# Performance work log

Measured on AMD Instinct MI355X. Metric: run time of the kernel, lower is better.

Reference implementation:

```python
import jax, jax.numpy as jnp
import numpy as np

B, N, D, H, DH = 128, 128, 64, 8, 64
CBS = SBS = 4
NSEL, WIN = 2, 2
NB = N // CBS
NEG = -1e30


def _ln(x, g, b, eps=1e-5):
    mu = jnp.mean(x, -1, keepdims=True)
    var = jnp.mean((x - mu) ** 2, -1, keepdims=True)
    return (x - mu) * jax.lax.rsqrt(var + eps) * g + b


def _rms(x, g, eps=1e-6):
    return x * jax.lax.rsqrt(jnp.mean(x * x, -1, keepdims=True) + eps) * g


def _gelu(x):
    return jax.nn.gelu(x, approximate=False)


def setup_inputs() -> dict:
    key = jax.random.key(0)
    ks = iter(jax.random.split(key, 40))
    def rn(shape, s=0.05):
        return jax.random.normal(next(ks), shape, jnp.float32) * s
    return dict(
        x=jax.random.normal(next(ks), (B, N), jnp.float32),
        W_emb=rn((D,)), b_emb=rn((D,)),
        rms_scale=jnp.ones((D,), jnp.float32),
        Wq=rn((D, H * DH)), Wk=rn((D, H * DH)), Wv=rn((D, H * DH)),
        k_pos=rn((H, CBS, DH)), v_pos=rn((H, CBS, DH)),
        Wck=rn((CBS * DH, DH)), bck=rn((DH,)), Wcv=rn((CBS * DH, DH)), bcv=rn((DH,)),
        mem_ck=rn((H, 1, DH)), mem_cv=rn((H, 1, DH)),
        Wg=rn((D, 3 * H)), bg=rn((3 * H,)),
        Wo=rn((H * DH, D)),
        ln1_g=jnp.ones((D,), jnp.float32), ln1_b=jnp.zeros((D,), jnp.float32),
        Wt1=rn((N, 256)), bt1=rn((256,)), Wt2=rn((256, N)), bt2=rn((N,)),
        ln2_g=jnp.ones((D,), jnp.float32), ln2_b=jnp.zeros((D,), jnp.float32),
        Wc1=rn((D, 256)), bc1=rn((256,)), Wc2=rn((256, D)), bc2=rn((D,)),
        Wh1=rn((D, 32)), bh1=rn((32,)), Wh2=rn((32, 1)), bh2=rn((1,)),
    )


def reference(x, W_emb, b_emb, rms_scale, Wq, Wk, Wv, k_pos, v_pos, Wck, bck, Wcv, bcv,
              mem_ck, mem_cv, Wg, bg, Wo, ln1_g, ln1_b, Wt1, bt1, Wt2, bt2,
              ln2_g, ln2_b, Wc1, bc1, Wc2, bc2, Wh1, bh1, Wh2, bh2):
    scale = DH ** -0.5
    pos = jnp.arange(N)
    e = x[..., None] * W_emb + b_emb                         # [B,N,D] per-feature embedding (Linear(1,D))
    # ---- NSA sparse attention branch ----
    h = _rms(e, rms_scale)
    q = (h @ Wq).reshape(B, N, H, DH).transpose(0, 2, 1, 3)  # bhnd
    k = (h @ Wk).reshape(B, N, H, DH).transpose(0, 2, 1, 3)
    v = (h @ Wv).reshape(B, N, H, DH).transpose(0, 2, 1, 3)
    # compressed-block branch: intra-block pos emb + linear compression, 1 learned mem KV
    kb = k.reshape(B, H, NB, CBS, DH) + k_pos[None, :, None]
    vb = v.reshape(B, H, NB, CBS, DH) + v_pos[None, :, None]
    ck = kb.reshape(B, H, NB, CBS * DH) @ Wck + bck          # [B,H,NB,DH]
    cv = vb.reshape(B, H, NB, CBS * DH) @ Wcv + bcv
    ckm = jnp.concatenate([jnp.broadcast_to(mem_ck[None], (B, H, 1, DH)), ck], axis=2)
    cvm = jnp.concatenate([jnp.broadcast_to(mem_cv[None], (B, H, 1, DH)), cv], axis=2)
    cs = jnp.einsum('bhnd,bhjd->bhnj', q, ckm) * scale
    blk_end = (jnp.arange(NB) + 1) * CBS - 1                 # block fully in the past is visible
    cmask = jnp.concatenate([jnp.ones((N, 1), bool), pos[:, None] >= blk_end[None, :]], axis=1)
    cs = jnp.where(cmask[None, None], cs, NEG)
    out_c = jnp.einsum('bhnj,bhjd->bhnd', jax.nn.softmax(cs, -1), cvm)
    # fine branch: top-k selected blocks (by compressed scores) + forced causal diagonal block
    vals, sel = jax.lax.top_k(cs[..., 1:], NSEL)             # [B,H,N,NSEL]
    qblk = pos // SBS
    sel_ok = (vals > NEG / 2) & (sel != qblk[None, None, :, None])
    sel_tok = (sel[..., None] * SBS + jnp.arange(SBS)).reshape(B, H, N, NSEL * SBS)
    gather = jax.vmap(jax.vmap(lambda t, i: t[i]))           # per (b,h) token gather
    fk_sel = gather(k, sel_tok)
    fv_sel = gather(v, sel_tok)
    diag = qblk[:, None] * SBS + jnp.arange(SBS)             # [N,SBS]
    fk = jnp.concatenate([fk_sel, k[:, :, diag]], axis=3)    # [B,H,N,(NSEL+1)*SBS,DH]
    fv = jnp.concatenate([fv_sel, v[:, :, diag]], axis=3)
    fidx = jnp.concatenate([sel_tok, jnp.broadcast_to(diag[None, None], (B, H, N, SBS))], axis=3)
    fmask = (fidx <= pos[None, None, :, None]) & jnp.concatenate(
        [jnp.repeat(sel_ok, SBS, axis=-1), jnp.ones((B, H, N, SBS), bool)], axis=3)
    fs = jnp.where(fmask, jnp.einsum('bhnd,bhnsd->bhns', q, fk) * scale, NEG)
    out_f = jnp.einsum('bhns,bhnsd->bhnd', jax.nn.softmax(fs, -1), fv)
    offs = pos[:, None] - jnp.arange(WIN - 1, -1, -1)[None, :]
    oc = jnp.clip(offs, 0, None)
    wk = k[:, :, oc]
    wv = v[:, :, oc]
    ws = jnp.where((offs >= 0)[None, None], jnp.einsum('bhnd,bhnwd->bhnw', q, wk) * scale, NEG)
    out_w = jnp.einsum('bhnw,bhnwd->bhnd', jax.nn.softmax(ws, -1), wv)
    # per-head sigmoid 3-way strategy gates + output projection
    g = jax.nn.sigmoid(h @ Wg + bg).reshape(B, N, 3, H).transpose(0, 3, 2, 1)  # [B,H,3,N]
    attn = g[:, :, 0, :, None] * out_c + g[:, :, 1, :, None] * out_f + g[:, :, 2, :, None] * out_w
    x1 = attn.transpose(0, 2, 1, 3).reshape(B, N, H * DH) @ Wo
    # ---- TabMixer branch (token-mix over N, channel-mix over D) ----
    t = _ln(e, ln1_g, ln1_b).transpose(0, 2, 1)              # [B,D,N]
    m = e + (_gelu(t @ Wt1 + bt1) @ Wt2 + bt2).transpose(0, 2, 1)
    m = m + _gelu(_ln(m, ln2_g, ln2_b) @ Wc1 + bc1) @ Wc2 + bc2
    # ---- fuse, mean-pool over tokens, MLP head ----
    y = (x1 + m).mean(axis=1)
    return _gelu(y @ Wh1 + bh1) @ Wh2 + bh2                  # [B,1]
```

## Files before the change

kernel.cpp:

```cpp
#include <hip/hip_runtime.h>
#include <math.h>

#define B_ 128
#define N_ 128
#define D_ 64
#define H_ 8
#define DH_ 64
#define NEGF (-1e30f)

__device__ __forceinline__ float wred(float v) {
#pragma unroll
  for (int off = 32; off > 0; off >>= 1) v += __shfl_xor(v, off, 64);
  return v;
}

__device__ __forceinline__ float gelu_f(float x) {
  return 0.5f * x * (1.f + erff(x * 0.70710678118654752440f));
}

__global__ void __launch_bounds__(256) k2_embed_proj(
    const float* __restrict__ x, const float* __restrict__ Wemb,
    const float* __restrict__ bemb, const float* __restrict__ rmsg,
    const float* __restrict__ ln1g, const float* __restrict__ ln1b,
    const float* __restrict__ Wq, const float* __restrict__ Wk,
    const float* __restrict__ Wv, const float* __restrict__ Wg,
    const float* __restrict__ bg, float* __restrict__ e,
    float* __restrict__ lne, float* __restrict__ q,
    float* __restrict__ k, float* __restrict__ v, float* __restrict__ g) {
  __shared__ __align__(16) float hs[32 * 68];
  int tid = threadIdx.x;
  int r0 = blockIdx.x * 32;
  int chunk = blockIdx.y;
  int wave = tid >> 6, lane = tid & 63;
  for (int rr = 0; rr < 8; ++rr) {
    int r = wave * 8 + rr;
    int row = r0 + r;
    float xv = x[row];
    float ev = fmaf(xv, Wemb[lane], bemb[lane]);
    float ss = wred(ev * ev) * (1.f / 64.f);
    float hv = ev * rsqrtf(ss + 1e-6f) * rmsg[lane];
    float mu = wred(ev) * (1.f / 64.f);
    float dv = ev - mu;
    float var = wred(dv * dv) * (1.f / 64.f);
    if (chunk == 0) {
      float lv = dv * rsqrtf(var + 1e-5f) * ln1g[lane] + ln1b[lane];
      size_t o = (size_t)row * 64 + lane;
      e[o] = ev; lne[o] = lv;
    }
    hs[r * 68 + lane] = hv;
  }
  __syncthreads();
  const float* W = (chunk == 0) ? Wq : ((chunk == 1) ? Wk : Wv);
  float* dst = (chunk == 0) ? q : ((chunk == 1) ? k : v);
  {
    int tx = tid & 127, ty = tid >> 7;
    float4 acc[16];
#pragma unroll
    for (int r = 0; r < 16; ++r) acc[r] = make_float4(0.f, 0.f, 0.f, 0.f);
    const float* Wp = W + 4 * tx;
#pragma unroll 2
    for (int k4 = 0; k4 < 16; ++k4) {
      float4 w0 = *(const float4*)(Wp + (size_t)(4 * k4 + 0) * 512);
      float4 w1 = *(const float4*)(Wp + (size_t)(4 * k4 + 1) * 512);
      float4 w2 = *(const float4*)(Wp + (size_t)(4 * k4 + 2) * 512);
      float4 w3 = *(const float4*)(Wp + (size_t)(4 * k4 + 3) * 512);
#pragma unroll
      for (int r = 0; r < 16; ++r) {
        float4 hv = *(const float4*)&hs[(ty * 16 + r) * 68 + 4 * k4];
        acc[r].x = fmaf(hv.x, w0.x, fmaf(hv.y, w1.x, fmaf(hv.z, w2.x, fmaf(hv.w, w3.x, acc[r].x))));
        acc[r].y = fmaf(hv.x, w0.y, fmaf(hv.y, w1.y, fmaf(hv.z, w2.y, fmaf(hv.w, w3.y, acc[r].y))));
        acc[r].z = fmaf(hv.x, w0.z, fmaf(hv.y, w1.z, fmaf(hv.z, w2.z, fmaf(hv.w, w3.z, acc[r].z))));
        acc[r].w = fmaf(hv.x, w0.w, fmaf(hv.y, w1.w, fmaf(hv.z, w2.w, fmaf(hv.w, w3.w, acc[r].w))));
      }
    }
    int hh = (4 * tx) >> 6, d4 = (4 * tx) & 63;
    int bb = r0 >> 7;
    float* dbase = dst + ((size_t)(bb * 8 + hh) * 128) * 64 + d4;
#pragma unroll
    for (int r = 0; r < 16; ++r) {
      int nn = (r0 & 127) + ty * 16 + r;
      *(float4*)(dbase + (size_t)nn * 64) = acc[r];
    }
  }
  {
    int r = tid >> 3, gl = tid & 7;
    int gc = chunk * 8 + gl;
    float a = bg[gc];
#pragma unroll 4
    for (int k4 = 0; k4 < 16; ++k4) {
      float4 hv = *(const float4*)&hs[r * 68 + 4 * k4];
      a = fmaf(hv.x, Wg[(4 * k4 + 0) * 24 + gc],
          fmaf(hv.y, Wg[(4 * k4 + 1) * 24 + gc],
          fmaf(hv.z, Wg[(4 * k4 + 2) * 24 + gc],
          fmaf(hv.w, Wg[(4 * k4 + 3) * 24 + gc], a))));
    }
    g[(size_t)(r0 + r) * 24 + gc] = 1.f / (1.f + __expf(-a));
  }
}

__global__ void __launch_bounds__(256) k3_compress(
    const float* __restrict__ k, const float* __restrict__ v,
    const float* __restrict__ kpos, const float* __restrict__ vpos,
    const float* __restrict__ Wck, const float* __restrict__ bck,
    const float* __restrict__ Wcv, const float* __restrict__ bcv,
    const float* __restrict__ mck, const float* __restrict__ mcv,
    float* __restrict__ ckm, float* __restrict__ cvm) {
  __shared__ __align__(16) float sb[32 * 260];
  int bh = blockIdx.x; int hh = bh & 7;
  int tid = threadIdx.x;
  int tx = tid & 15, ty = tid >> 4;
  const float4* sb4 = (const float4*)sb;
  for (int pass = 0; pass < 2; ++pass) {
    const float* src = pass ? v : k;
    const float* pos = pass ? vpos : kpos;
    const float* Wc = pass ? Wcv : Wck;
    const float* bc = pass ? bcv : bck;
    const float* mc = pass ? mcv : mck;
    float* out = pass ? cvm : ckm;
    if (pass) __syncthreads();
    for (int idx = tid; idx < 8192; idx += 256) {
      int tok = idx >> 6, dd = idx & 63;
      sb[(tok >> 2) * 260 + (tok & 3) * 64 + dd] =
          src[(size_t)bh * 8192 + idx] + pos[(hh * 4 + (tok & 3)) * 64 + dd];
    }
    __syncthreads();
    float4 b4 = *(const float4*)(bc + 4 * tx);
    float4 a0 = b4, a1 = b4;
    const float* Wp = Wc + 4 * tx;
#pragma unroll 2
    for (int k4 = 0; k4 < 64; ++k4) {
      float4 w0 = *(const float4*)(Wp + (size_t)(4 * k4 + 0) * 64);
      float4 w1 = *(const float4*)(Wp + (size_t)(4 * k4 + 1) * 64);
      float4 w2 = *(const float4*)(Wp + (size_t)(4 * k4 + 2) * 64);
      float4 w3 = *(const float4*)(Wp + (size_t)(4 * k4 + 3) * 64);
      float4 s0 = sb4[ty * 65 + k4];
      float4 s1 = sb4[(ty + 16) * 65 + k4];
      a0.x = fmaf(s0.x, w0.x, fmaf(s0.y, w1.x, fmaf(s0.z, w2.x, fmaf(s0.w, w3.x, a0.x))));
      a0.y = fmaf(s0.x, w0.y, fmaf(s0.y, w1.y, fmaf(s0.z, w2.y, fmaf(s0.w, w3.y, a0.y))));
      a0.z = fmaf(s0.x, w0.z, fmaf(s0.y, w1.z, fmaf(s0.z, w2.z, fmaf(s0.w, w3.z, a0.z))));
      a0.w = fmaf(s0.x, w0.w, fmaf(s0.y, w1.w, fmaf(s0.z, w2.w, fmaf(s0.w, w3.w, a0.w))));
      a1.x = fmaf(s1.x, w0.x, fmaf(s1.y, w1.x, fmaf(s1.z, w2.x, fmaf(s1.w, w3.x, a1.x))));
      a1.y = fmaf(s1.x, w0.y, fmaf(s1.y, w1.y, fmaf(s1.z, w2.y, fmaf(s1.w, w3.y, a1.y))));
      a1.z = fmaf(s1.x, w0.z, fmaf(s1.y, w1.z, fmaf(s1.z, w2.z, fmaf(s1.w, w3.z, a1.z))));
      a1.w = fmaf(s1.x, w0.w, fmaf(s1.y, w1.w, fmaf(s1.z, w2.w, fmaf(s1.w, w3.w, a1.w))));
    }
    *(float4*)(out + ((size_t)bh * 33 + ty + 1) * 64 + 4 * tx) = a0;
    *(float4*)(out + ((size_t)bh * 33 + ty + 17) * 64 + 4 * tx) = a1;
    if (tid < 16) *(float4*)(out + (size_t)bh * 2112 + 4 * tid) = *(const float4*)(mc + hh * 64 + 4 * tid);
  }
}

#define KLD 68
__global__ void __launch_bounds__(128, 2) k4_attn(
    const float* __restrict__ q, const float* __restrict__ k, const float* __restrict__ v,
    const float* __restrict__ ckm, const float* __restrict__ cvm, const float* __restrict__ g,
    float* __restrict__ attn) {
  __shared__ __align__(16) float ks[128 * KLD];
  int bh = blockIdx.x; int b = bh >> 3, hh = bh & 7;
  int tid = threadIdx.x;
  for (int idx = tid; idx < 8192; idx += 128)
    ks[(idx >> 6) * KLD + (idx & 63)] = k[(size_t)bh * 8192 + idx];
  __syncthreads();
  const int n = tid;
  float4 qr[16];
  {
    const float4* q4 = (const float4*)(q + (size_t)bh * 8192 + (size_t)n * 64);
#pragma unroll
    for (int i = 0; i < 16; ++i) {
      float4 t = q4[i];
      t.x *= 0.125f; t.y *= 0.125f; t.z *= 0.125f; t.w *= 0.125f;
      qr[i] = t;
    }
  }
  auto dot = [&](const float4* __restrict__ rp) {
    float s0 = 0.f, s1 = 0.f;
#pragma unroll
    for (int i = 0; i < 16; i += 2) {
      float4 c0 = rp[i], c1 = rp[i + 1];
      s0 = fmaf(qr[i].x, c0.x, s0); s0 = fmaf(qr[i].y, c0.y, s0);
      s0 = fmaf(qr[i].z, c0.z, s0); s0 = fmaf(qr[i].w, c0.w, s0);
      s1 = fmaf(qr[i + 1].x, c1.x, s1); s1 = fmaf(qr[i + 1].y, c1.y, s1);
      s1 = fmaf(qr[i + 1].z, c1.z, s1); s1 = fmaf(qr[i + 1].w, c1.w, s1);
    }
    return s0 + s1;
  };
  const float* ck0 = ckm + (size_t)bh * 2112;
  const int jmax = (n + 1) >> 2;
  float scc[33];
#pragma unroll
  for (int j = 0; j < 33; ++j) {
    float s = dot((const float4*)(ck0 + j * 64));
    scc[j] = (j == 0 || j <= jmax) ? s : NEGF;
  }
  int i1 = 0; float b1 = scc[1];
#pragma unroll
  for (int j = 2; j < 33; ++j) {
    if (scc[j] > b1) { b1 = scc[j]; i1 = j - 1; }
  }
  int i2 = 0; float b2 = -3.0e38f;
#pragma unroll
  for (int j = 1; j < 33; ++j) {
    if ((j - 1 != i1) && (scc[j] > b2)) { b2 = scc[j]; i2 = j - 1; }
  }
  const int qb = n >> 2;
  const bool ok1 = (b1 > -5e29f) && (i1 != qb);
  const bool ok2 = (b2 > -5e29f) && (i2 != qb);
  const int row1 = i1 * 4, row2 = i2 * 4, rowd = qb * 4;
  float sf[12];
#pragma unroll
  for (int s2 = 0; s2 < 4; ++s2) {
    int t1 = row1 + s2;
    sf[s2] = (ok1 && t1 <= n) ? dot((const float4*)(ks + t1 * KLD)) : NEGF;
    int t2 = row2 + s2;
    sf[4 + s2] = (ok2 && t2 <= n) ? dot((const float4*)(ks + t2 * KLD)) : NEGF;
    int t3 = rowd + s2;
    sf[8 + s2] = (t3 <= n) ? dot((const float4*)(ks + t3 * KLD)) : NEGF;
  }
  float sw0 = (n >= 1) ? dot((const float4*)(ks + (n - 1) * KLD)) : NEGF;
  float sw1 = dot((const float4*)(ks + n * KLD));
  __syncthreads();
  for (int idx = tid; idx < 8192; idx += 128)
    ks[(idx >> 6) * KLD + (idx & 63)] = v[(size_t)bh * 8192 + idx];
  __syncthreads();
  float mxc = scc[0];
#pragma unroll
  for (int j = 1; j < 33; ++j) mxc = fmaxf(mxc, scc[j]);
  float denc = 0.f;
#pragma unroll
  for (int j = 0; j < 33; ++j) { float p = __expf(scc[j] - mxc); scc[j] = p; denc += p; }
  float mxf = sf[0];
#pragma unroll
  for (int i = 1; i < 12; ++i) mxf = fmaxf(mxf, sf[i]);
  float denf = 0.f;
#pragma unroll
  for (int i = 0; i < 12; ++i) { float p = __expf(sf[i] - mxf); sf[i] = p; denf += p; }
  float mxw = fmaxf(sw0, sw1);
  float pw0 = __expf(sw0 - mxw), pw1 = __expf(sw1 - mxw);
  const float* gr = g + (size_t)(b * 128 + n) * 24;
  float gc0 = gr[hh] / denc;
  float gf0 = gr[8 + hh] / denf;
  float gw0 = gr[16 + hh] / (pw0 + pw1);
  float pww0 = pw0 * gw0, pww1 = pw1 * gw0;
  int nm1 = (n >= 1) ? (n - 1) : 0;
  const float* cv0 = cvm + (size_t)bh * 2112;
  float4* arow = (float4*)(attn + ((size_t)(b * 128 + n)) * 512 + hh * 64);
  for (int h2 = 0; h2 < 2; ++h2) {
    float4 oa[8];
#pragma unroll
    for (int i = 0; i < 8; ++i) oa[i] = make_float4(0.f, 0.f, 0.f, 0.f);
#pragma unroll
    for (int j = 0; j < 33; ++j) {
      float p = scc[j] * gc0;
      const float4* cr = (const float4*)(cv0 + j * 64) + h2 * 8;
#pragma unroll
      for (int i = 0; i < 8; ++i) {
        float4 c = cr[i];
        oa[i].x = fmaf(p, c.x, oa[i].x); oa[i].y = fmaf(p, c.y, oa[i].y);
        oa[i].z = fmaf(p, c.z, oa[i].z); oa[i].w = fmaf(p, c.w, oa[i].w);
      }
    }
#pragma unroll
    for (int si = 0; si < 12; ++si) {
      int tok = ((si < 4) ? row1 : (si < 8) ? row2 : rowd) + (si & 3);
      float p = sf[si] * gf0;
      const float4* vr = (const float4*)(ks + tok * KLD) + h2 * 8;
#pragma unroll
      for (int i = 0; i < 8; ++i) {
        float4 c = vr[i];
        oa[i].x = fmaf(p, c.x, oa[i].x); oa[i].y = fmaf(p, c.y, oa[i].y);
        oa[i].z = fmaf(p, c.z, oa[i].z); oa[i].w = fmaf(p, c.w, oa[i].w);
      }
    }
    {
      const float4* v0 = (const float4*)(ks + nm1 * KLD) + h2 * 8;
      const float4* v1 = (const float4*)(ks + n * KLD) + h2 * 8;
#pragma unroll
      for (int i = 0; i < 8; ++i) {
        float4 c0 = v0[i], c1 = v1[i];
        oa[i].x = fmaf(pww0, c0.x, fmaf(pww1, c1.x, oa[i].x));
        oa[i].y = fmaf(pww0, c0.y, fmaf(pww1, c1.y, oa[i].y));
        oa[i].z = fmaf(pww0, c0.z, fmaf(pww1, c1.z, oa[i].z));
        oa[i].w = fmaf(pww0, c0.w, fmaf(pww1, c1.w, oa[i].w));
      }
    }
#pragma unroll
    for (int i = 0; i < 8; ++i) arow[h2 * 8 + i] = oa[i];
  }
}

__global__ void __launch_bounds__(256) k5_wo(const float* __restrict__ attn,
                                             const float* __restrict__ Wo,
                                             float* __restrict__ x1) {
  __shared__ __align__(16) float as[16 * 516];
  int tid = threadIdx.x;
  size_t base = (size_t)blockIdx.x * 8192;
  for (int idx = tid; idx < 8192; idx += 256)
    as[(idx >> 9) * 516 + (idx & 511)] = attn[base + idx];
  __syncthreads();
  int tx = tid & 15, ty = tid >> 4;
  const float4* as4 = (const float4*)as;
  float4 acc = make_float4(0.f, 0.f, 0.f, 0.f);
  const float* Wp = Wo + 4 * tx;
#pragma unroll 4
  for (int k4 = 0; k4 < 128; ++k4) {
    float4 w0 = *(const float4*)(Wp + (size_t)(4 * k4 + 0) * 64);
    float4 w1 = *(const float4*)(Wp + (size_t)(4 * k4 + 1) * 64);
    float4 w2 = *(const float4*)(Wp + (size_t)(4 * k4 + 2) * 64);
    float4 w3 = *(const float4*)(Wp + (size_t)(4 * k4 + 3) * 64);
    float4 a = as4[ty * 129 + k4];
    acc.x = fmaf(a.x, w0.x, fmaf(a.y, w1.x, fmaf(a.z, w2.x, fmaf(a.w, w3.x, acc.x))));
    acc.y = fmaf(a.x, w0.y, fmaf(a.y, w1.y, fmaf(a.z, w2.y, fmaf(a.w, w3.y, acc.y))));
    acc.z = fmaf(a.x, w0.z, fmaf(a.y, w1.z, fmaf(a.z, w2.z, fmaf(a.w, w3.z, acc.z))));
    acc.w = fmaf(a.x, w0.w, fmaf(a.y, w1.w, fmaf(a.z, w2.w, fmaf(a.w, w3.w, acc.w))));
  }
  *(float4*)(x1 + ((size_t)blockIdx.x * 16 + ty) * 64 + 4 * tx) = acc;
}

__global__ void __launch_bounds__(256) k6_token(
    const float* __restrict__ lne, const float* __restrict__ e,
    const float* __restrict__ Wt1, const float* __restrict__ bt1,
    const float* __restrict__ Wt2, const float* __restrict__ bt2,
    float* __restrict__ m) {
  __shared__ __align__(16) float trow[4 * 132];
  __shared__ __align__(16) float hid[4 * 260];
  int b = blockIdx.x >> 4, d0 = (blockIdx.x & 15) * 4;
  int tid = threadIdx.x;
  for (int idx = tid; idx < 512; idx += 256) {
    int nn = idx >> 2, dl = idx & 3;
    trow[dl * 132 + nn] = lne[((size_t)b * 128 + nn) * 64 + d0 + dl];
  }
  __syncthreads();
  {
    int tx = tid & 63, ty = tid >> 6;
    float4 acc = *(const float4*)(bt1 + 4 * tx);
    const float4* tr4 = (const float4*)&trow[ty * 132];
    const float* Wp = Wt1 + 4 * tx;
#pragma unroll 2
    for (int k4 = 0; k4 < 32; ++k4) {
      float4 w0 = *(const float4*)(Wp + (size_t)(4 * k4 + 0) * 256);
      float4 w1 = *(const float4*)(Wp + (size_t)(4 * k4 + 1) * 256);
      float4 w2 = *(const float4*)(Wp + (size_t)(4 * k4 + 2) * 256);
      float4 w3 = *(const float4*)(Wp + (size_t)(4 * k4 + 3) * 256);
      float4 t = tr4[k4];
      acc.x = fmaf(t.x, w0.x, fmaf(t.y, w1.x, fmaf(t.z, w2.x, fmaf(t.w, w3.x, acc.x))));
      acc.y = fmaf(t.x, w0.y, fmaf(t.y, w1.y, fmaf(t.z, w2.y, fmaf(t.w, w3.y, acc.y))));
      acc.z = fmaf(t.x, w0.z, fmaf(t.y, w1.z, fmaf(t.z, w2.z, fmaf(t.w, w3.z, acc.z))));
      acc.w = fmaf(t.x, w0.w, fmaf(t.y, w1.w, fmaf(t.z, w2.w, fmaf(t.w, w3.w, acc.w))));
    }
    float* hp = &hid[ty * 260 + 4 * tx];
    hp[0] = gelu_f(acc.x); hp[1] = gelu_f(acc.y); hp[2] = gelu_f(acc.z); hp[3] = gelu_f(acc.w);
  }
  __syncthreads();
  {
    int tx = tid & 63, ty = tid >> 6;
    float o0 = bt2[2 * tx], o1 = bt2[2 * tx + 1];
    const float4* h4 = (const float4*)&hid[ty * 260];
    const float* Wp = Wt2 + 2 * tx;
#pragma unroll 2
    for (int k4 = 0; k4 < 64; ++k4) {
      float2 w0 = *(const float2*)(Wp + (size_t)(4 * k4 + 0) * 128);
      float2 w1 = *(const float2*)(Wp + (size_t)(4 * k4 + 1) * 128);
      float2 w2 = *(const float2*)(Wp + (size_t)(4 * k4 + 2) * 128);
      float2 w3 = *(const float2*)(Wp + (size_t)(4 * k4 + 3) * 128);
      float4 t = h4[k4];
      o0 = fmaf(t.x, w0.x, fmaf(t.y, w1.x, fmaf(t.z, w2.x, fmaf(t.w, w3.x, o0))));
      o1 = fmaf(t.x, w0.y, fmaf(t.y, w1.y, fmaf(t.z, w2.y, fmaf(t.w, w3.y, o1))));
    }
    size_t oi0 = ((size_t)b * 128 + 2 * tx) * 64 + d0 + ty;
    size_t oi1 = oi0 + 64;
    m[oi0] = e[oi0] + o0;
    m[oi1] = e[oi1] + o1;
  }
}

__global__ void __launch_bounds__(256) k7_channel(
    float* __restrict__ m, const float* __restrict__ g2, const float* __restrict__ b2,
    const float* __restrict__ Wc1, const float* __restrict__ bc1,
    const float* __restrict__ Wc2, const float* __restrict__ bc2) {
  __shared__ __align__(16) float lnr[8 * 68];
  __shared__ __align__(16) float hid[8 * 260];
  int tid = threadIdx.x;
  int wv = tid >> 6, lane = tid & 63;
  size_t r0 = (size_t)blockIdx.x * 8;
  for (int rr = 0; rr < 2; ++rr) {
    int r = wv * 2 + rr;
    float mv = m[(r0 + r) * 64 + lane];
    float mu = wred(mv) * (1.f / 64.f);
    float dv = mv - mu;
    float var = wred(dv * dv) * (1.f / 64.f);
    lnr[r * 68 + lane] = dv * rsqrtf(var + 1e-5f) * g2[lane] + b2[lane];
  }
  __syncthreads();
  {
    int tx = tid & 63, ty = tid >> 6;
    float4 b4 = *(const float4*)(bc1 + 4 * tx);
    float4 a0 = b4, a1 = b4;
    const float4* l0 = (const float4*)&lnr[ty * 68];
    const float4* l1 = (const float4*)&lnr[(ty + 4) * 68];
    const float* Wp = Wc1 + 4 * tx;
#pragma unroll 2
    for (int k4 = 0; k4 < 16; ++k4) {
      float4 w0 = *(const float4*)(Wp + (size_t)(4 * k4 + 0) * 256);
      float4 w1 = *(const float4*)(Wp + (size_t)(4 * k4 + 1) * 256);
      float4 w2 = *(const float4*)(Wp + (size_t)(4 * k4 + 2) * 256);
      float4 w3 = *(const float4*)(Wp + (size_t)(4 * k4 + 3) * 256);
      float4 s0 = l0[k4], s1 = l1[k4];
      a0.x = fmaf(s0.x, w0.x, fmaf(s0.y, w1.x, fmaf(s0.z, w2.x, fmaf(s0.w, w3.x, a0.x))));
      a0.y = fmaf(s0.x, w0.y, fmaf(s0.y, w1.y, fmaf(s0.z, w2.y, fmaf(s0.w, w3.y, a0.y))));
      a0.z = fmaf(s0.x, w0.z, fmaf(s0.y, w1.z, fmaf(s0.z, w2.z, fmaf(s0.w, w3.z, a0.z))));
      a0.w = fmaf(s0.x, w0.w, fmaf(s0.y, w1.w, fmaf(s0.z, w2.w, fmaf(s0.w, w3.w, a0.w))));
      a1.x = fmaf(s1.x, w0.x, fmaf(s1.y, w1.x, fmaf(s1.z, w2.x, fmaf(s1.w, w3.x, a1.x))));
      a1.y = fmaf(s1.x, w0.y, fmaf(s1.y, w1.y, fmaf(s1.z, w2.y, fmaf(s1.w, w3.y, a1.y))));
      a1.z = fmaf(s1.x, w0.z, fmaf(s1.y, w1.z, fmaf(s1.z, w2.z, fmaf(s1.w, w3.z, a1.z))));
      a1.w = fmaf(s1.x, w0.w, fmaf(s1.y, w1.w, fmaf(s1.z, w2.w, fmaf(s1.w, w3.w, a1.w))));
    }
    float* h0 = &hid[ty * 260 + 4 * tx];
    float* h1 = &hid[(ty + 4) * 260 + 4 * tx];
    h0[0] = gelu_f(a0.x); h0[1] = gelu_f(a0.y); h0[2] = gelu_f(a0.z); h0[3] = gelu_f(a0.w);
    h1[0] = gelu_f(a1.x); h1[1] = gelu_f(a1.y); h1[2] = gelu_f(a1.z); h1[3] = gelu_f(a1.w);
  }
  __syncthreads();
  {
    int tx = tid & 31, ty = tid >> 5;
    float o0 = bc2[2 * tx], o1 = bc2[2 * tx + 1];
    const float4* h4 = (const float4*)&hid[ty * 260];
    const float* Wp = Wc2 + 2 * tx;
#pragma unroll 2
    for (int k4 = 0; k4 < 64; ++k4) {
      float2 w0 = *(const float2*)(Wp + (size_t)(4 * k4 + 0) * 64);
      float2 w1 = *(const float2*)(Wp + (size_t)(4 * k4 + 1) * 64);
      float2 w2 = *(const float2*)(Wp + (size_t)(4 * k4 + 2) * 64);
      float2 w3 = *(const float2*)(Wp + (size_t)(4 * k4 + 3) * 64);
      float4 t = h4[k4];
      o0 = fmaf(t.x, w0.x, fmaf(t.y, w1.x, fmaf(t.z, w2.x, fmaf(t.w, w3.x, o0))));
      o1 = fmaf(t.x, w0.y, fmaf(t.y, w1.y, fmaf(t.z, w2.y, fmaf(t.w, w3.y, o1))));
    }
    size_t oi = (r0 + ty) * 64 + 2 * tx;
    m[oi] = m[oi] + o0;
    m[oi + 1] = m[oi + 1] + o1;
  }
}

__global__ void __launch_bounds__(256) k8_head(
    const float* __restrict__ x1, const float* __restrict__ m,
    const float* __restrict__ Wh1, const float* __restrict__ bh1,
    const float* __restrict__ Wh2, const float* __restrict__ bh2,
    float* __restrict__ out) {
  __shared__ float ysp[4 * 64];
  __shared__ float ys[64];
  int b = blockIdx.x, tid = threadIdx.x;
  int qtr = tid >> 6, lane = tid & 63;
  float acc = 0.f;
  for (int nn = qtr * 32; nn < qtr * 32 + 32; ++nn) {
    size_t oi = ((size_t)b * 128 + nn) * 64 + lane;
    acc += x1[oi] + m[oi];
  }
  ysp[qtr * 64 + lane] = acc;
  __syncthreads();
  if (tid < 64) ys[tid] = (ysp[tid] + ysp[64 + tid] + ysp[128 + tid] + ysp[192 + tid]) * (1.f / 128.f);
  __syncthreads();
  if (tid < 64) {
    float partial = 0.f;
    if (tid < 32) {
      float a = bh1[tid];
      for (int dd = 0; dd < 64; ++dd) a = fmaf(ys[dd], Wh1[dd * 32 + tid], a);
      partial = gelu_f(a) * Wh2[tid];
    }
    partial = wred(partial);
    if (tid == 0) out[b] = partial + bh2[0];
  }
}

extern "C" void kernel_launch(void* const* d_in, const int* in_sizes, int n_in,
                              void* d_out, int out_size, void* d_ws, size_t ws_size,
                              hipStream_t stream) {
  const float* x     = (const float*)d_in[0];
  const float* Wemb  = (const float*)d_in[1];
  const float* bemb  = (const float*)d_in[2];
  const float* rmsg  = (const float*)d_in[3];
  const float* Wq    = (const float*)d_in[4];
  const float* Wk    = (const float*)d_in[5];
  const float* Wv    = (const float*)d_in[6];
  const float* kpos  = (const float*)d_in[7];
  const float* vpos  = (const float*)d_in[8];
  const float* Wck   = (const float*)d_in[9];
  const float* bck   = (const float*)d_in[10];
  const float* Wcv   = (const float*)d_in[11];
  const float* bcv   = (const float*)d_in[12];
  const float* mck   = (const float*)d_in[13];
  const float* mcv   = (const float*)d_in[14];
  const float* Wg    = (const float*)d_in[15];
  const float* bg    = (const float*)d_in[16];
  const float* Wo    = (const float*)d_in[17];
  const float* ln1g  = (const float*)d_in[18];
  const float* ln1b  = (const float*)d_in[19];
  const float* Wt1   = (const float*)d_in[20];
  const float* bt1   = (const float*)d_in[21];
  const float* Wt2   = (const float*)d_in[22];
  const float* bt2   = (const float*)d_in[23];
  const float* ln2g  = (const float*)d_in[24];
  const float* ln2b  = (const float*)d_in[25];
  const float* Wc1   = (const float*)d_in[26];
  const float* bc1   = (const float*)d_in[27];
  const float* Wc2   = (const float*)d_in[28];
  const float* bc2   = (const float*)d_in[29];
  const float* Wh1   = (const float*)d_in[30];
  const float* bh1   = (const float*)d_in[31];
  const float* Wh2   = (const float*)d_in[32];
  const float* bh2   = (const float*)d_in[33];

  float* ws = (float*)d_ws;
  const size_t SZ_ROWD = (size_t)B_ * N_ * D_;
  const size_t SZ_BHND = (size_t)B_ * H_ * N_ * DH_;
  float* e    = ws;
  float* lne  = e + SZ_ROWD;
  float* q    = lne + SZ_ROWD;
  float* k    = q + SZ_BHND;
  float* v    = k + SZ_BHND;
  float* g    = v + SZ_BHND;
  float* ckm  = g + (size_t)B_ * N_ * 24;
  float* cvm  = ckm + (size_t)B_ * H_ * 33 * 64;
  float* attn = cvm + (size_t)B_ * H_ * 33 * 64;
  float* x1   = k;
  float* m    = v;

  k2_embed_proj<<<dim3(B_ * N_ / 32, 3), dim3(256), 0, stream>>>(
      x, Wemb, bemb, rmsg, ln1g, ln1b, Wq, Wk, Wv, Wg, bg, e, lne, q, k, v, g);
  k3_compress<<<dim3(B_ * H_), dim3(256), 0, stream>>>(k, v, kpos, vpos, Wck, bck, Wcv, bcv, mck, mcv, ckm, cvm);
  k4_attn<<<dim3(B_ * H_), dim3(128), 0, stream>>>(q, k, v, ckm, cvm, g, attn);
  k5_wo<<<dim3(B_ * N_ / 16), dim3(256), 0, stream>>>(attn, Wo, x1);
  k6_token<<<dim3(B_ * 16), dim3(256), 0, stream>>>(lne, e, Wt1, bt1, Wt2, bt2, m);
  k7_channel<<<dim3(B_ * N_ / 8), dim3(256), 0, stream>>>(m, ln2g, ln2b, Wc1, bc1, Wc2, bc2);
  k8_head<<<dim3(B_), dim3(256), 0, stream>>>(x1, m, Wh1, bh1, Wh2, bh2, (float*)d_out);
}
```

Baseline: 568.8 us.

## Register-tile token and channel mixer MLPs over more rows per block

The token-mix kernel now handles 32 feature columns per block instead of 4, and the channel-mix kernel handles 32 rows instead of 8. Each thread accumulates 8, 4 or 2 output rows in registers, so each weight value fetched from global memory is reused across several rows. The token-mix output is staged back through shared memory so the final residual write to m is coalesced, and the channel-mix residual update uses float4. The cost is higher register and shared-memory use and far fewer blocks: 256 for token-mix, 512 for channel-mix.

```diff
diff --git a/kernel.cpp b/kernel.cpp
--- a/kernel.cpp
+++ b/kernel.cpp
@@ -321,19 +321,21 @@
     const float* __restrict__ Wt1, const float* __restrict__ bt1,
     const float* __restrict__ Wt2, const float* __restrict__ bt2,
     float* __restrict__ m) {
-  __shared__ __align__(16) float trow[4 * 132];
-  __shared__ __align__(16) float hid[4 * 260];
-  int b = blockIdx.x >> 4, d0 = (blockIdx.x & 15) * 4;
+  __shared__ __align__(16) float trow[32 * 132];
+  __shared__ __align__(16) float hid[32 * 260];
+  int b = blockIdx.x >> 1, d0 = (blockIdx.x & 1) * 32;
   int tid = threadIdx.x;
-  for (int idx = tid; idx < 512; idx += 256) {
-    int nn = idx >> 2, dl = idx & 3;
+  for (int idx = tid; idx < 4096; idx += 256) {
+    int dl = idx & 31, nn = idx >> 5;
     trow[dl * 132 + nn] = lne[((size_t)b * 128 + nn) * 64 + d0 + dl];
   }
   __syncthreads();
   {
     int tx = tid & 63, ty = tid >> 6;
-    float4 acc = *(const float4*)(bt1 + 4 * tx);
-    const float4* tr4 = (const float4*)&trow[ty * 132];
+    float4 bias = *(const float4*)(bt1 + 4 * tx);
+    float4 acc[8];
+#pragma unroll
+    for (int r = 0; r < 8; ++r) acc[r] = bias;
     const float* Wp = Wt1 + 4 * tx;
 #pragma unroll 2
     for (int k4 = 0; k4 < 32; ++k4) {
@@ -341,35 +343,54 @@
       float4 w1 = *(const float4*)(Wp + (size_t)(4 * k4 + 1) * 256);
       float4 w2 = *(const float4*)(Wp + (size_t)(4 * k4 + 2) * 256);
       float4 w3 = *(const float4*)(Wp + (size_t)(4 * k4 + 3) * 256);
-      float4 t = tr4[k4];
-      acc.x = fmaf(t.x, w0.x, fmaf(t.y, w1.x, fmaf(t.z, w2.x, fmaf(t.w, w3.x, acc.x))));
-      acc.y = fmaf(t.x, w0.y, fmaf(t.y, w1.y, fmaf(t.z, w2.y, fmaf(t.w, w3.y, acc.y))));
-      acc.z = fmaf(t.x, w0.z, fmaf(t.y, w1.z, fmaf(t.z, w2.z, fmaf(t.w, w3.z, acc.z))));
-      acc.w = fmaf(t.x, w0.w, fmaf(t.y, w1.w, fmaf(t.z, w2.w, fmaf(t.w, w3.w, acc.w))));
-    }
-    float* hp = &hid[ty * 260 + 4 * tx];
-    hp[0] = gelu_f(acc.x); hp[1] = gelu_f(acc.y); hp[2] = gelu_f(acc.z); hp[3] = gelu_f(acc.w);
-  }
-  __syncthreads();
-  {
-    int tx = tid & 63, ty = tid >> 6;
-    float o0 = bt2[2 * tx], o1 = bt2[2 * tx + 1];
-    const float4* h4 = (const float4*)&hid[ty * 260];
-    const float* Wp = Wt2 + 2 * tx;
+#pragma unroll
+      for (int r = 0; r < 8; ++r) {
+        float4 t = *(const float4*)&trow[(ty * 8 + r) * 132 + 4 * k4];
+        acc[r].x = fmaf(t.x, w0.x, fmaf(t.y, w1.x, fmaf(t.z, w2.x, fmaf(t.w, w3.x, acc[r].x))));
+        acc[r].y = fmaf(t.x, w0.y, fmaf(t.y, w1.y, fmaf(t.z, w2.y, fmaf(t.w, w3.y, acc[r].y))));
+        acc[r].z = fmaf(t.x, w0.z, fmaf(t.y, w1.z, fmaf(t.z, w2.z, fmaf(t.w, w3.z, acc[r].z))));
+        acc[r].w = fmaf(t.x, w0.w, fmaf(t.y, w1.w, fmaf(t.z, w2.w, fmaf(t.w, w3.w, acc[r].w))));
+      }
+    }
+#pragma unroll
+    for (int r = 0; r < 8; ++r) {
+      float* hp = &hid[(ty * 8 + r) * 260 + 4 * tx];
+      hp[0] = gelu_f(acc[r].x); hp[1] = gelu_f(acc[r].y);
+      hp[2] = gelu_f(acc[r].z); hp[3] = gelu_f(acc[r].w);
+    }
+  }
+  __syncthreads();
+  {
+    int tx = tid & 31, ty = tid >> 5;
+    float4 bias = *(const float4*)(bt2 + 4 * tx);
+    float4 acc[4];
+#pragma unroll
+    for (int r = 0; r < 4; ++r) acc[r] = bias;
+    const float* Wp = Wt2 + 4 * tx;
 #pragma unroll 2
     for (int k4 = 0; k4 < 64; ++k4) {
-      float2 w0 = *(const float2*)(Wp + (size_t)(4 * k4 + 0) * 128);
-      float2 w1 = *(const float2*)(Wp + (size_t)(4 * k4 + 1) * 128);
-      float2 w2 = *(const float2*)(Wp + (size_t)(4 * k4 + 2) * 128);
-      float2 w3 = *(const float2*)(Wp + (size_t)(4 * k4 + 3) * 128);
-      float4 t = h4[k4];
-      o0 = fmaf(t.x, w0.x, fmaf(t.y, w1.x, fmaf(t.z, w2.x, fmaf(t.w, w3.x, o0))));
-      o1 = fmaf(t.x, w0.y, fmaf(t.y, w1.y, fmaf(t.z, w2.y, fmaf(t.w, w3.y, o1))));
-    }
-    size_t oi0 = ((size_t)b * 128 + 2 * tx) * 64 + d0 + ty;
-    size_t oi1 = oi0 + 64;
-    m[oi0] = e[oi0] + o0;
-    m[oi1] = e[oi1] + o1;
+      float4 w0 = *(const float4*)(Wp + (size_t)(4 * k4 + 0) * 128);
+      float4 w1 = *(const float4*)(Wp + (size_t)(4 * k4 + 1) * 128);
+      float4 w2 = *(const float4*)(Wp + (size_t)(4 * k4 + 2) * 128);
+      float4 w3 = *(const float4*)(Wp + (size_t)(4 * k4 + 3) * 128);
+#pragma unroll
+      for (int r = 0; r < 4; ++r) {
+        float4 t = *(const float4*)&hid[(ty * 4 + r) * 260 + 4 * k4];
+        acc[r].x = fmaf(t.x, w0.x, fmaf(t.y, w1.x, fmaf(t.z, w2.x, fmaf(t.w, w3.x, acc[r].x))));
+        acc[r].y = fmaf(t.x, w0.y, fmaf(t.y, w1.y, fmaf(t.z, w2.y, fmaf(t.w, w3.y, acc[r].y))));
+        acc[r].z = fmaf(t.x, w0.z, fmaf(t.y, w1.z, fmaf(t.z, w2.z, fmaf(t.w, w3.z, acc[r].z))));
+        acc[r].w = fmaf(t.x, w0.w, fmaf(t.y, w1.w, fmaf(t.z, w2.w, fmaf(t.w, w3.w, acc[r].w))));
+      }
+    }
+#pragma unroll
+    for (int r = 0; r < 4; ++r)
+      *(float4*)&trow[(ty * 4 + r) * 132 + 4 * tx] = acc[r];
+  }
+  __syncthreads();
+  for (int idx = tid; idx < 4096; idx += 256) {
+    int dl = idx & 31, nn = idx >> 5;
+    size_t oi = ((size_t)b * 128 + nn) * 64 + d0 + dl;
+    m[oi] = e[oi] + trow[dl * 132 + nn];
   }
 }
 
@@ -377,13 +398,13 @@
     float* __restrict__ m, const float* __restrict__ g2, const float* __restrict__ b2,
     const float* __restrict__ Wc1, const float* __restrict__ bc1,
     const float* __restrict__ Wc2, const float* __restrict__ bc2) {
-  __shared__ __align__(16) float lnr[8 * 68];
-  __shared__ __align__(16) float hid[8 * 260];
+  __shared__ __align__(16) float lnr[32 * 68];
+  __shared__ __align__(16) float hid[32 * 260];
   int tid = threadIdx.x;
   int wv = tid >> 6, lane = tid & 63;
-  size_t r0 = (size_t)blockIdx.x * 8;
-  for (int rr = 0; rr < 2; ++rr) {
-    int r = wv * 2 + rr;
+  size_t r0 = (size_t)blockIdx.x * 32;
+  for (int rr = 0; rr < 8; ++rr) {
+    int r = wv * 8 + rr;
     float mv = m[(r0 + r) * 64 + lane];
     float mu = wred(mv) * (1.f / 64.f);
     float dv = mv - mu;
@@ -393,10 +414,10 @@
   __syncthreads();
   {
     int tx = tid & 63, ty = tid >> 6;
-    float4 b4 = *(const float4*)(bc1 + 4 * tx);
-    float4 a0 = b4, a1 = b4;
-    const float4* l0 = (const float4*)&lnr[ty * 68];
-    const float4* l1 = (const float4*)&lnr[(ty + 4) * 68];
+    float4 bias = *(const float4*)(bc1 + 4 * tx);
+    float4 acc[8];
+#pragma unroll
+    for (int r = 0; r < 8; ++r) acc[r] = bias;
     const float* Wp = Wc1 + 4 * tx;
 #pragma unroll 2
     for (int k4 = 0; k4 < 16; ++k4) {
@@ -404,40 +425,52 @@
       float4 w1 = *(const float4*)(Wp + (size_t)(4 * k4 + 1) * 256);
       float4 w2 = *(const float4*)(Wp + (size_t)(4 * k4 + 2) * 256);
       float4 w3 = *(const float4*)(Wp + (size_t)(4 * k4 + 3) * 256);
-      float4 s0 = l0[k4], s1 = l1[k4];
-      a0.x = fmaf(s0.x, w0.x, fmaf(s0.y, w1.x, fmaf(s0.z, w2.x, fmaf(s0.w, w3.x, a0.x))));
-      a0.y = fmaf(s0.x, w0.y, fmaf(s0.y, w1.y, fmaf(s0.z, w2.y, fmaf(s0.w, w3.y, a0.y))));
-      a0.z = fmaf(s0.x, w0.z, fmaf(s0.y, w1.z, fmaf(s0.z, w2.z, fmaf(s0.w, w3.z, a0.z))));
-      a0.w = fmaf(s0.x, w0.w, fmaf(s0.y, w1.w, fmaf(s0.z, w2.w, fmaf(s0.w, w3.w, a0.w))));
-      a1.x = fmaf(s1.x, w0.x, fmaf(s1.y, w1.x, fmaf(s1.z, w2.x, fmaf(s1.w, w3.x, a1.x))));
-      a1.y = fmaf(s1.x, w0.y, fmaf(s1.y, w1.y, fmaf(s1.z, w2.y, fmaf(s1.w, w3.y, a1.y))));
-      a1.z = fmaf(s1.x, w0.z, fmaf(s1.y, w1.z, fmaf(s1.z, w2.z, fmaf(s1.w, w3.z, a1.z))));
-      a1.w = fmaf(s1.x, w0.w, fmaf(s1.y, w1.w, fmaf(s1.z, w2.w, fmaf(s1.w, w3.w, a1.w))));
-    }
-    float* h0 = &hid[ty * 260 + 4 * tx];
-    float* h1 = &hid[(ty + 4) * 260 + 4 * tx];
-    h0[0] = gelu_f(a0.x); h0[1] = gelu_f(a0.y); h0[2] = gelu_f(a0.z); h0[3] = gelu_f(a0.w);
-    h1[0] = gelu_f(a1.x); h1[1] = gelu_f(a1.y); h1[2] = gelu_f(a1.z); h1[3] = gelu_f(a1.w);
-  }
-  __syncthreads();
-  {
-    int tx = tid & 31, ty = tid >> 5;
-    float o0 = bc2[2 * tx], o1 = bc2[2 * tx + 1];
-    const float4* h4 = (const float4*)&hid[ty * 260];
-    const float* Wp = Wc2 + 2 * tx;
+#pragma unroll
+      for (int r = 0; r < 8; ++r) {
+        float4 t = *(const float4*)&lnr[(ty * 8 + r) * 68 + 4 * k4];
+        acc[r].x = fmaf(t.x, w0.x, fmaf(t.y, w1.x, fmaf(t.z, w2.x, fmaf(t.w, w3.x, acc[r].x))));
+        acc[r].y = fmaf(t.x, w0.y, fmaf(t.y, w1.y, fmaf(t.z, w2.y, fmaf(t.w, w3.y, acc[r].y))));
+        acc[r].z = fmaf(t.x, w0.z, fmaf(t.y, w1.z, fmaf(t.z, w2.z, fmaf(t.w, w3.z, acc[r].z))));
+        acc[r].w = fmaf(t.x, w0.w, fmaf(t.y, w1.w, fmaf(t.z, w2.w, fmaf(t.w, w3.w, acc[r].w))));
+      }
+    }
+#pragma unroll
+    for (int r = 0; r < 8; ++r) {
+      float* hp = &hid[(ty * 8 + r) * 260 + 4 * tx];
+      hp[0] = gelu_f(acc[r].x); hp[1] = gelu_f(acc[r].y);
+      hp[2] = gelu_f(acc[r].z); hp[3] = gelu_f(acc[r].w);
+    }
+  }
+  __syncthreads();
+  {
+    int tx = tid & 15, ty = tid >> 4;
+    float4 bias = *(const float4*)(bc2 + 4 * tx);
+    float4 acc[2];
+#pragma unroll
+    for (int r = 0; r < 2; ++r) acc[r] = bias;
+    const float* Wp = Wc2 + 4 * tx;
 #pragma unroll 2
     for (int k4 = 0; k4 < 64; ++k4) {
-      float2 w0 = *(const float2*)(Wp + (size_t)(4 * k4 + 0) * 64);
-      float2 w1 = *(const float2*)(Wp + (size_t)(4 * k4 + 1) * 64);
-      float2 w2 = *(const float2*)(Wp + (size_t)(4 * k4 + 2) * 64);
-      float2 w3 = *(const float2*)(Wp + (size_t)(4 * k4 + 3) * 64);
-      float4 t = h4[k4];
-      o0 = fmaf(t.x, w0.x, fmaf(t.y, w1.x, fmaf(t.z, w2.x, fmaf(t.w, w3.x, o0))));
-      o1 = fmaf(t.x, w0.y, fmaf(t.y, w1.y, fmaf(t.z, w2.y, fmaf(t.w, w3.y, o1))));
-    }
-    size_t oi = (r0 + ty) * 64 + 2 * tx;
-    m[oi] = m[oi] + o0;
-    m[oi + 1] = m[oi + 1] + o1;
+      float4 w0 = *(const float4*)(Wp + (size_t)(4 * k4 + 0) * 64);
+      float4 w1 = *(const float4*)(Wp + (size_t)(4 * k4 + 1) * 64);
+      float4 w2 = *(const float4*)(Wp + (size_t)(4 * k4 + 2) * 64);
+      float4 w3 = *(const float4*)(Wp + (size_t)(4 * k4 + 3) * 64);
+#pragma unroll
+      for (int r = 0; r < 2; ++r) {
+        float4 t = *(const float4*)&hid[(ty * 2 + r) * 260 + 4 * k4];
+        acc[r].x = fmaf(t.x, w0.x, fmaf(t.y, w1.x, fmaf(t.z, w2.x, fmaf(t.w, w3.x, acc[r].x))));
+        acc[r].y = fmaf(t.x, w0.y, fmaf(t.y, w1.y, fmaf(t.z, w2.y, fmaf(t.w, w3.y, acc[r].y))));
+        acc[r].z = fmaf(t.x, w0.z, fmaf(t.y, w1.z, fmaf(t.z, w2.z, fmaf(t.w, w3.z, acc[r].z))));
+        acc[r].w = fmaf(t.x, w0.w, fmaf(t.y, w1.w, fmaf(t.z, w2.w, fmaf(t.w, w3.w, acc[r].w))));
+      }
+    }
+#pragma unroll
+    for (int r = 0; r < 2; ++r) {
+      float4* mp = (float4*)(m + (r0 + ty * 2 + r) * 64 + 4 * tx);
+      float4 old = *mp;
+      old.x += acc[r].x; old.y += acc[r].y; old.z += acc[r].z; old.w += acc[r].w;
+      *mp = old;
+    }
   }
 }
 
@@ -529,7 +562,7 @@
   k3_compress<<<dim3(B_ * H_), dim3(256), 0, stream>>>(k, v, kpos, vpos, Wck, bck, Wcv, bcv, mck, mcv, ckm, cvm);
   k4_attn<<<dim3(B_ * H_), dim3(128), 0, stream>>>(q, k, v, ckm, cvm, g, attn);
   k5_wo<<<dim3(B_ * N_ / 16), dim3(256), 0, stream>>>(attn, Wo, x1);
-  k6_token<<<dim3(B_ * 16), dim3(256), 0, stream>>>(lne, e, Wt1, bt1, Wt2, bt2, m);
-  k7_channel<<<dim3(B_ * N_ / 8), dim3(256), 0, stream>>>(m, ln2g, ln2b, Wc1, bc1, Wc2, bc2);
+  k6_token<<<dim3(B_ * 2), dim3(256), 0, stream>>>(lne, e, Wt1, bt1, Wt2, bt2, m);
+  k7_channel<<<dim3(B_ * N_ / 32), dim3(256), 0, stream>>>(m, ln2g, ln2b, Wc1, bc1, Wc2, bc2);
   k8_head<<<dim3(B_), dim3(256), 0, stream>>>(x1, m, Wh1, bh1, Wh2, bh2, (float*)d_out);
 }
```

Measured after the change: 460.9 us. -19.0%, faster.
